# Kernel tuning notes

Measured on AMD Instinct MI355X. Metric: run time of the kernel, lower is better.

The kernel has to match this reference:

```python
import jax, jax.numpy as jnp
import numpy as np

D, E, K, H = 512, 8, 2, 128   # input_dim, num_experts, top-k, expert hidden (Expert default)
CAPF = 1.25                    # capacity_factor
N = 32768                      # tokens


def setup_inputs() -> dict:
    key = jax.random.key(0)
    ks = jax.random.split(key, 6)
    s = 0.02
    return {
        "x":  jax.random.normal(ks[0], (N, D), jnp.float32),
        "Wr": jax.random.normal(ks[1], (D, E), jnp.float32) * s,   # router linear weight
        "br": jnp.zeros((E,), jnp.float32),
        "W1": jax.random.normal(ks[2], (E, D, H), jnp.float32) * s,  # expert first linear (stacked)
        "b1": jnp.zeros((E, H), jnp.float32),
        "W2": jax.random.normal(ks[3], (E, H, D), jnp.float32) * s,  # expert second linear (stacked)
        "b2": jnp.zeros((E, D), jnp.float32),
    }


def reference(x, Wr, br, W1, b1, W2, b2):
    n = x.shape[0]
    # ---- router (eval mode: no noise, temperature=1) ----
    logits = x @ Wr + br                                   # [N, E]
    topk_vals, topk_idx = jax.lax.top_k(logits, K)         # [N, K]
    gates_k = jax.nn.softmax(topk_vals, axis=-1)
    rows = jnp.arange(n)[:, None]
    sparse_gates = jnp.zeros_like(logits).at[rows, topk_idx].set(gates_k)  # [N, E]
    confidence = topk_vals.max(axis=-1).mean()
    # ---- capacity-limited dispatch (keep first `cap` routed tokens per expert) ----
    cap = int(CAPF * (n / E))
    mask = sparse_gates > 0                                # [N, E] routed mask
    pos = jnp.cumsum(mask, axis=0) - 1                     # rank of token within expert queue
    keep = mask & (pos < cap)                              # [N, E]
    load = keep.sum(axis=0).astype(x.dtype)                # [E]
    # ---- per-expert 2-layer FFN over all tokens, combined with keep mask ----
    # (original adds expert output un-weighted by gates to kept token positions)
    h = jax.nn.relu(jnp.einsum('nd,edh->enh', x, W1) + b1[:, None, :])   # [E, N, H]
    y = jnp.einsum('enh,ehd->end', h, W2) + b2[:, None, :]               # [E, N, D]
    out = jnp.einsum('ne,end->nd', keep.astype(x.dtype), y)             # [N, D]
    # ---- load-balance stats ----
    load_dist = load / (load.sum() + 1e-8)
    load_loss = (load_dist * jnp.log(load_dist + 1e-8)).sum()
    return out, load_loss, load_dist, confidence
```

## Files before the change

### kernel.cpp

```cpp
#include <hip/hip_runtime.h>

#define D 512
#define E 8
#define H 128
#define BM 64
#define HP 136
#define RT 16

typedef __attribute__((ext_vector_type(8))) short short8v;
typedef __attribute__((ext_vector_type(4))) short short4v;
typedef __attribute__((ext_vector_type(4))) float float4v;

__device__ inline short f2bf(float f) {
  union { float f; unsigned u; } v; v.f = f;
  unsigned r = v.u + 0x7fffu + ((v.u >> 16) & 1u);
  return (short)(r >> 16);
}
__device__ inline float bf2f(short s) {
  union { unsigned u; float f; } v;
  v.u = ((unsigned)(unsigned short)s) << 16;
  return v.f;
}
__device__ inline void gload_lds4(const void* g, void* l) {
  __builtin_amdgcn_global_load_lds(
      (const __attribute__((address_space(1))) unsigned int*)g,
      (__attribute__((address_space(3))) unsigned int*)l, 4, 0, 0);
}

__global__ void k_swizzle(const float* __restrict__ W1, const float* __restrict__ W2,
                          short* __restrict__ W1f, short* __restrict__ W2f) {
  const int e = blockIdx.y;
  const int lane = threadIdx.x & 63;
  const int wv = threadIdx.x >> 6;
  const int r = lane & 15, g = lane >> 4;
  const int which = blockIdx.x >> 4;
  const int fbase = ((blockIdx.x & 15) * 4 + wv) * 2;
  if (which == 0) {
#pragma unroll
    for (int f = fbase; f < fbase + 2; ++f) {
      int ks = f >> 3, t = f & 7;
      const float* src = W1 + ((size_t)e * D + ks * 32 + g * 8) * H + t * 16 + r;
      short8v o;
#pragma unroll
      for (int j = 0; j < 8; ++j) o[j] = f2bf(src[(size_t)j * H]);
      *(short8v*)(W1f + (((size_t)e * 128 + f) * 64 + lane) * 8) = o;
    }
  } else {
#pragma unroll
    for (int f = fbase; f < fbase + 2; ++f) {
      int t = f >> 2, ks = f & 3;
      const float* src = W2 + ((size_t)e * H + ks * 32 + g * 8) * D + t * 16 + r;
      short8v o;
#pragma unroll
      for (int j = 0; j < 8; ++j) o[j] = f2bf(src[(size_t)j * D]);
      *(short8v*)(W2f + (((size_t)e * 128 + f) * 64 + lane) * 8) = o;
    }
  }
}

__global__ void k_router(const float* __restrict__ x, const float* __restrict__ Wr,
                         const float* __restrict__ br, int* __restrict__ tokE,
                         float* __restrict__ confPart, short* __restrict__ xb) {
  const int lane = threadIdx.x & 63;
  const int wave = threadIdx.x >> 6;
  const int tbase = (blockIdx.x * 4 + wave) * RT;

  float wr[8][8];
  const float4* wrp = reinterpret_cast<const float4*>(Wr) + lane * 16;
#pragma unroll
  for (int j = 0; j < 8; ++j) {
    float4 a = wrp[j * 2 + 0];
    float4 b = wrp[j * 2 + 1];
    wr[j][0] = a.x; wr[j][1] = a.y; wr[j][2] = a.z; wr[j][3] = a.w;
    wr[j][4] = b.x; wr[j][5] = b.y; wr[j][6] = b.z; wr[j][7] = b.w;
  }

  const int myE = ((lane & 1) << 2) | (lane & 2) | ((lane >> 2) & 1);
  const float brv = br[myE];

  float conf = 0.f;

#pragma unroll 2
  for (int tt = 0; tt < RT; ++tt) {
    const int token = tbase + tt;
    const float4* xp = reinterpret_cast<const float4*>(x + (size_t)token * D + lane * 8);
    float4 x0 = xp[0], x1 = xp[1];
    float xv[8] = {x0.x, x0.y, x0.z, x0.w, x1.x, x1.y, x1.z, x1.w};

    if (xb) {
      short8v p;
#pragma unroll
      for (int j = 0; j < 8; ++j) p[j] = f2bf(xv[j]);
      *(short8v*)(xb + (size_t)token * D + lane * 8) = p;
    }

    float v[8] = {0, 0, 0, 0, 0, 0, 0, 0};
#pragma unroll
    for (int j = 0; j < 8; ++j)
#pragma unroll
      for (int e = 0; e < E; ++e)
        v[e] += xv[j] * wr[j][e];

#pragma unroll
    for (int i = 0; i < 4; ++i) {
      float a = v[i] + __shfl_xor(v[i], 1, 64);
      float b = v[i + 4] + __shfl_xor(v[i + 4], 1, 64);
      v[i] = (lane & 1) ? b : a;
    }
#pragma unroll
    for (int i = 0; i < 2; ++i) {
      float a = v[i] + __shfl_xor(v[i], 2, 64);
      float b = v[i + 2] + __shfl_xor(v[i + 2], 2, 64);
      v[i] = (lane & 2) ? b : a;
    }
    {
      float a = v[0] + __shfl_xor(v[0], 4, 64);
      float b = v[1] + __shfl_xor(v[1], 4, 64);
      v[0] = (lane & 4) ? b : a;
    }
    v[0] += __shfl_xor(v[0], 8, 64);
    v[0] += __shfl_xor(v[0], 16, 64);
    v[0] += __shfl_xor(v[0], 32, 64);

    const float logit = v[0] + brv;

    float m1 = logit; int i1 = myE;
#pragma unroll
    for (int m = 1; m <= 4; m <<= 1) {
      float om = __shfl_xor(m1, m, 64);
      int oi = __shfl_xor(i1, m, 64);
      bool take = (om > m1) || (om == m1 && oi < i1);
      m1 = take ? om : m1;
      i1 = take ? oi : i1;
    }
    float s1 = (myE == i1) ? -1e30f : logit; int j1 = myE;
#pragma unroll
    for (int m = 1; m <= 4; m <<= 1) {
      float om = __shfl_xor(s1, m, 64);
      int oi = __shfl_xor(j1, m, 64);
      bool take = (om > s1) || (om == s1 && oi < j1);
      s1 = take ? om : s1;
      j1 = take ? oi : j1;
    }

    if (lane == 0) {
      tokE[token * 2 + 0] = i1;
      tokE[token * 2 + 1] = j1;
    }
    conf += m1;
  }

  __shared__ float cf[4];
  if (lane == 0) cf[wave] = conf;
  __syncthreads();
  if (threadIdx.x == 0) confPart[blockIdx.x] = cf[0] + cf[1] + cf[2] + cf[3];
}

__global__ void k_count(const int* __restrict__ tokE, int* __restrict__ chunkCnt) {
  __shared__ int c[E];
  if (threadIdx.x < E) c[threadIdx.x] = 0;
  __syncthreads();
  int token = blockIdx.x * 256 + threadIdx.x;
  atomicAdd(&c[tokE[token * 2 + 0]], 1);
  atomicAdd(&c[tokE[token * 2 + 1]], 1);
  __syncthreads();
  if (threadIdx.x < E) chunkCnt[blockIdx.x * E + threadIdx.x] = c[threadIdx.x];
}

__global__ void k_scan(const int* __restrict__ chunkCnt, const float* __restrict__ confPart,
                       int* __restrict__ chunkOff, int* __restrict__ kept,
                       float* __restrict__ outTail, int nConf, int cap, int nTok) {
  const int lane = threadIdx.x & 63;
  const int e = threadIdx.x >> 6;
  __shared__ int keptS[E];

  int v0 = chunkCnt[lane * E + e];
  int v1 = chunkCnt[(64 + lane) * E + e];
  int s0 = v0, s1 = v1;
#pragma unroll
  for (int off = 1; off < 64; off <<= 1) {
    int t0 = __shfl_up(s0, off, 64);
    int t1 = __shfl_up(s1, off, 64);
    if (lane >= off) { s0 += t0; s1 += t1; }
  }
  int tot0 = __shfl(s0, 63, 64);
  int total = tot0 + __shfl(s1, 63, 64);
  chunkOff[lane * E + e] = s0 - v0;
  chunkOff[(64 + lane) * E + e] = tot0 + s1 - v1;
  if (lane == 0) {
    int k = min(total, cap);
    kept[e] = k;
    keptS[e] = k;
  }

  __shared__ float s[512];
  float a = 0.f;
  for (int i = threadIdx.x; i < nConf; i += 512) a += confPart[i];
  s[threadIdx.x] = a;
  __syncthreads();
  for (int st = 256; st > 0; st >>= 1) {
    if (threadIdx.x < st) s[threadIdx.x] += s[threadIdx.x + st];
    __syncthreads();
  }
  if (threadIdx.x == 0) {
    float tot = 0.f, ld[E];
    for (int i = 0; i < E; ++i) { ld[i] = (float)keptS[i]; tot += ld[i]; }
    float denom = tot + 1e-8f;
    float loss = 0.f;
    for (int i = 0; i < E; ++i) {
      float dist = ld[i] / denom;
      loss += dist * logf(dist + 1e-8f);
      outTail[1 + i] = dist;
    }
    outTail[0] = loss;
    outTail[1 + E] = s[0] / (float)nTok;
  }
}

__global__ void k_dispatch(const int* __restrict__ tokE, const int* __restrict__ chunkOff,
                           int* __restrict__ expList, int2* __restrict__ tokSlot, int cap) {
  const int lane = threadIdx.x & 63;
  const int wave = threadIdx.x >> 6;
  const int token = blockIdx.x * 256 + threadIdx.x;
  const int e0 = tokE[token * 2 + 0];
  const int e1 = tokE[token * 2 + 1];
  __shared__ int wcnt[4][E];
  unsigned long long lt = (lane == 63) ? 0x7fffffffffffffffull : ((1ull << lane) - 1ull);
  int r0 = 0, r1 = 0;
#pragma unroll
  for (int e = 0; e < E; ++e) {
    unsigned long long b0 = __ballot(e0 == e);
    unsigned long long b1 = __ballot(e1 == e);
    unsigned long long m = b0 | b1;
    if (e0 == e) r0 = __popcll(m & lt);
    if (e1 == e) r1 = __popcll(m & lt);
    if (lane == 0) wcnt[wave][e] = __popcll(m);
  }
  __syncthreads();
  int base0 = chunkOff[blockIdx.x * E + e0];
  int base1 = chunkOff[blockIdx.x * E + e1];
  for (int w = 0; w < wave; ++w) {
    base0 += wcnt[w][e0];
    base1 += wcnt[w][e1];
  }
  int g0 = base0 + r0;
  int g1 = base1 + r1;
  if (g0 < cap) expList[e0 * cap + g0] = token;
  if (g1 < cap) expList[e1 * cap + g1] = token;
  tokSlot[token] = make_int2(g0 < cap ? e0 * cap + g0 : -1,
                             g1 < cap ? e1 * cap + g1 : -1);
}

template <bool USE_XB>
__global__ __launch_bounds__(256) void k_expert_mfma(
    const short* __restrict__ xb, const float* __restrict__ x,
    const short* __restrict__ W1f, const float* __restrict__ b1,
    const short* __restrict__ W2f, const float* __restrict__ b2,
    const int* __restrict__ expList, const int* __restrict__ kept,
    short* __restrict__ yscr, int cap) {
  const int e = blockIdx.y;
  const int cnt = kept[e];
  const int t0 = blockIdx.x * BM;
  if (t0 >= cnt) return;
  const int lane = threadIdx.x & 63;
  const int wave = threadIdx.x >> 6;
  const int rb = wave * 16;
  const int n15 = lane & 15;
  const int grp = lane >> 4;
  const int kg = grp * 8;

  __shared__ int toks[BM];
  __shared__ short sbuf[2 * BM * HP];

  if (threadIdx.x < BM) {
    int idx = min(t0 + (int)threadIdx.x, cnt - 1);
    toks[threadIdx.x] = expList[e * cap + idx];
  }
  __syncthreads();

  const short* w1 = W1f + (size_t)e * (128 * 512);
  const short* w2 = W2f + (size_t)e * (128 * 512);

  float4v acc[8];
#pragma unroll
  for (int t = 0; t < 8; ++t) acc[t] = (float4v){0.f, 0.f, 0.f, 0.f};

  if (USE_XB) {
    auto stageX = [&](int p) {
#pragma unroll
      for (int j = 0; j < 16; ++j) {
        int ti = wave * 16 + j;
        const short* src = xb + (size_t)toks[ti] * D + p * 128 + lane * 2;
        short* dst = &sbuf[(p & 1) * (BM * HP) + ti * HP];
        gload_lds4(src, dst);
      }
    };
    stageX(0);
    __syncthreads();
#pragma unroll
    for (int p = 0; p < 4; ++p) {
      if (p < 3) stageX(p + 1);
#pragma unroll
      for (int ksl = 0; ksl < 4; ++ksl) {
        const int ks = p * 4 + ksl;
        short8v xf = *(const short8v*)&sbuf[(p & 1) * (BM * HP) +
                                            (rb + n15) * HP + ksl * 32 + kg];
        short8v wf[8];
#pragma unroll
        for (int t = 0; t < 8; ++t)
          wf[t] = *(const short8v*)(w1 + (size_t)(ks * 8 + t) * 512 + lane * 8);
#pragma unroll
        for (int t = 0; t < 8; ++t)
          acc[t] = __builtin_amdgcn_mfma_f32_16x16x32_bf16(wf[t], xf, acc[t], 0, 0, 0);
      }
      __syncthreads();
    }
  } else {
    const float* xrowF = x + (size_t)toks[rb + n15] * D + kg;
    short8v xf[16];
#pragma unroll
    for (int ks = 0; ks < 16; ++ks) {
      float4 a = *(const float4*)(xrowF + ks * 32);
      float4 b = *(const float4*)(xrowF + ks * 32 + 4);
      short8v f;
      f[0] = f2bf(a.x); f[1] = f2bf(a.y); f[2] = f2bf(a.z); f[3] = f2bf(a.w);
      f[4] = f2bf(b.x); f[5] = f2bf(b.y); f[6] = f2bf(b.z); f[7] = f2bf(b.w);
      xf[ks] = f;
    }
#pragma unroll
    for (int ks = 0; ks < 16; ++ks) {
      short8v wf[8];
#pragma unroll
      for (int t = 0; t < 8; ++t)
        wf[t] = *(const short8v*)(w1 + (size_t)(ks * 8 + t) * 512 + lane * 8);
#pragma unroll
      for (int t = 0; t < 8; ++t)
        acc[t] = __builtin_amdgcn_mfma_f32_16x16x32_bf16(wf[t], xf[ks], acc[t], 0, 0, 0);
    }
    __syncthreads();
  }

  short* hrow = &sbuf[(rb + n15) * HP];
#pragma unroll
  for (int t = 0; t < 8; ++t) {
    float4 bb = *(const float4*)(b1 + e * H + t * 16 + grp * 4);
    short4v p;
    p[0] = f2bf(fmaxf(acc[t][0] + bb.x, 0.f));
    p[1] = f2bf(fmaxf(acc[t][1] + bb.y, 0.f));
    p[2] = f2bf(fmaxf(acc[t][2] + bb.z, 0.f));
    p[3] = f2bf(fmaxf(acc[t][3] + bb.w, 0.f));
    *(short4v*)(hrow + t * 16 + grp * 4) = p;
  }
  __syncthreads();

  short8v a4[4];
#pragma unroll
  for (int ks = 0; ks < 4; ++ks)
    a4[ks] = *(const short8v*)(&sbuf[(rb + n15) * HP + ks * 32 + kg]);

  short* yrow = yscr + ((size_t)(e * cap + t0 + rb + n15)) * D;
#pragma unroll 4
  for (int t = 0; t < 32; ++t) {
    short8v wf[4];
#pragma unroll
    for (int ks = 0; ks < 4; ++ks)
      wf[ks] = *(const short8v*)(w2 + (size_t)(t * 4 + ks) * 512 + lane * 8);
    float4v y = (float4v){0.f, 0.f, 0.f, 0.f};
#pragma unroll
    for (int ks = 0; ks < 4; ++ks)
      y = __builtin_amdgcn_mfma_f32_16x16x32_bf16(wf[ks], a4[ks], y, 0, 0, 0);
    float4 bb = *(const float4*)(b2 + e * D + t * 16 + grp * 4);
    short4v p;
    p[0] = f2bf(y[0] + bb.x);
    p[1] = f2bf(y[1] + bb.y);
    p[2] = f2bf(y[2] + bb.z);
    p[3] = f2bf(y[3] + bb.w);
    *(short4v*)(yrow + t * 16 + grp * 4) = p;
  }
}

__global__ void k_combine(const short* __restrict__ yscr, const int2* __restrict__ tokSlot,
                          float* __restrict__ out) {
  const int idx = blockIdx.x * 256 + threadIdx.x;
  const int token = idx >> 7;
  const int c4 = idx & 127;
  int2 sl = tokSlot[token];
  float4 r = make_float4(0.f, 0.f, 0.f, 0.f);
  if (sl.x >= 0) {
    short4v y = *(const short4v*)(yscr + (size_t)sl.x * D + c4 * 4);
    r.x += bf2f(y[0]); r.y += bf2f(y[1]); r.z += bf2f(y[2]); r.w += bf2f(y[3]);
  }
  if (sl.y >= 0) {
    short4v y = *(const short4v*)(yscr + (size_t)sl.y * D + c4 * 4);
    r.x += bf2f(y[0]); r.y += bf2f(y[1]); r.z += bf2f(y[2]); r.w += bf2f(y[3]);
  }
  reinterpret_cast<float4*>(out)[idx] = r;
}

extern "C" void kernel_launch(void* const* d_in, const int* in_sizes, int n_in,
                              void* d_out, int out_size, void* d_ws, size_t ws_size,
                              hipStream_t stream) {
  const float* x  = (const float*)d_in[0];
  const float* Wr = (const float*)d_in[1];
  const float* br = (const float*)d_in[2];
  const float* W1 = (const float*)d_in[3];
  const float* b1 = (const float*)d_in[4];
  const float* W2 = (const float*)d_in[5];
  const float* b2 = (const float*)d_in[6];
  float* out = (float*)d_out;

  const int N = in_sizes[0] / D;
  const int cap = (int)(1.25f * (float)(N / E));
  const int chunks = N / 256;
  const int rblocks = N / (4 * RT);

  int* tokE = (int*)d_ws;
  float* confPart = (float*)(tokE + (size_t)N * 2);
  int* chunkCnt = (int*)(confPart + rblocks);
  int* chunkOff = chunkCnt + chunks * E;
  int* kept = chunkOff + chunks * E;
  int2* tokSlot = (int2*)(kept + E);
  int* expList = (int*)(tokSlot + N);
  short* W1f = (short*)(expList + (size_t)E * cap);
  short* W2f = W1f + (size_t)E * H * D;
  short* yscr = W2f + (size_t)E * H * D;
  short* xb = yscr + (size_t)E * cap * D;

  const size_t needed = (size_t)((char*)(xb + (size_t)N * D) - (char*)d_ws);
  const bool useXB = ws_size >= needed;

  k_swizzle<<<dim3(32, E), 256, 0, stream>>>(W1, W2, W1f, W2f);

  k_router<<<rblocks, 256, 0, stream>>>(x, Wr, br, tokE, confPart,
                                        useXB ? xb : nullptr);
  k_count<<<chunks, 256, 0, stream>>>(tokE, chunkCnt);
  k_scan<<<1, 512, 0, stream>>>(chunkCnt, confPart, chunkOff, kept,
                                out + (size_t)N * D, rblocks, cap, N);
  k_dispatch<<<chunks, 256, 0, stream>>>(tokE, chunkOff, expList, tokSlot, cap);

  const int tiles = (cap + BM - 1) / BM;
  dim3 g5(tiles, E);
  if (useXB)
    k_expert_mfma<true><<<g5, 256, 0, stream>>>(xb, x, W1f, b1, W2f, b2,
                                                expList, kept, yscr, cap);
  else
    k_expert_mfma<false><<<g5, 256, 0, stream>>>(nullptr, x, W1f, b1, W2f, b2,
                                                 expList, kept, yscr, cap);

  k_combine<<<(N * D / 4) / 256, 256, 0, stream>>>(yscr, tokSlot, out);
}
```

Before: 113.3 us.

## Enlarge expert tile to 128 tokens with a 2x4 wave grid for weight reuse

The expert FFN kernel now processes 128 tokens per block with 512 threads. The 8 waves form a 2x4 grid: each wave covers 64 rows and a quarter of the hidden/output columns. Each W1/W2 fragment loaded from global is therefore reused across several 16-row tiles, cutting weight traffic per token. The trade-off is half as many blocks (fewer than two per CU), a larger LDS footprint and one-block-per-CU launch bounds, so occupancy and latency hiding may suffer. RT is also changed for the router stage.

```diff
diff --git a/kernel.cpp b/kernel.cpp
--- a/kernel.cpp
+++ b/kernel.cpp
@@ -3,9 +3,9 @@
 #define D 512
 #define E 8
 #define H 128
-#define BM 64
+#define BM 128
 #define HP 136
-#define RT 16
+#define RT 8
 
 typedef __attribute__((ext_vector_type(8))) short short8v;
 typedef __attribute__((ext_vector_type(4))) short short4v;
@@ -252,7 +252,7 @@
 }
 
 template <bool USE_XB>
-__global__ __launch_bounds__(256) void k_expert_mfma(
+__global__ __launch_bounds__(512, 1) void k_expert_mfma(
     const short* __restrict__ xb, const float* __restrict__ x,
     const short* __restrict__ W1f, const float* __restrict__ b1,
     const short* __restrict__ W2f, const float* __restrict__ b2,
@@ -264,7 +264,8 @@
   if (t0 >= cnt) return;
   const int lane = threadIdx.x & 63;
   const int wave = threadIdx.x >> 6;
-  const int rb = wave * 16;
+  const int rowg = wave >> 2;
+  const int ng = wave & 3;
   const int n15 = lane & 15;
   const int grp = lane >> 4;
   const int kg = grp * 8;
@@ -281,9 +282,12 @@
   const short* w1 = W1f + (size_t)e * (128 * 512);
   const short* w2 = W2f + (size_t)e * (128 * 512);
 
-  float4v acc[8];
-#pragma unroll
-  for (int t = 0; t < 8; ++t) acc[t] = (float4v){0.f, 0.f, 0.f, 0.f};
+  float4v acc[4][2];
+#pragma unroll
+  for (int r = 0; r < 4; ++r)
+#pragma unroll
+    for (int t = 0; t < 2; ++t)
+      acc[r][t] = (float4v){0.f, 0.f, 0.f, 0.f};
 
   if (USE_XB) {
     auto stageX = [&](int p) {
@@ -303,79 +307,105 @@
 #pragma unroll
       for (int ksl = 0; ksl < 4; ++ksl) {
         const int ks = p * 4 + ksl;
-        short8v xf = *(const short8v*)&sbuf[(p & 1) * (BM * HP) +
-                                            (rb + n15) * HP + ksl * 32 + kg];
-        short8v wf[8];
-#pragma unroll
-        for (int t = 0; t < 8; ++t)
-          wf[t] = *(const short8v*)(w1 + (size_t)(ks * 8 + t) * 512 + lane * 8);
-#pragma unroll
-        for (int t = 0; t < 8; ++t)
-          acc[t] = __builtin_amdgcn_mfma_f32_16x16x32_bf16(wf[t], xf, acc[t], 0, 0, 0);
+        const short* sb = &sbuf[(p & 1) * (BM * HP)];
+        short8v xf[4];
+#pragma unroll
+        for (int r = 0; r < 4; ++r)
+          xf[r] = *(const short8v*)&sb[(rowg * 64 + r * 16 + n15) * HP + ksl * 32 + kg];
+        short8v wf[2];
+#pragma unroll
+        for (int t = 0; t < 2; ++t)
+          wf[t] = *(const short8v*)(w1 + (size_t)(ks * 8 + ng * 2 + t) * 512 + lane * 8);
+#pragma unroll
+        for (int t = 0; t < 2; ++t)
+#pragma unroll
+          for (int r = 0; r < 4; ++r)
+            acc[r][t] = __builtin_amdgcn_mfma_f32_16x16x32_bf16(wf[t], xf[r], acc[r][t], 0, 0, 0);
       }
       __syncthreads();
     }
   } else {
-    const float* xrowF = x + (size_t)toks[rb + n15] * D + kg;
-    short8v xf[16];
-#pragma unroll
+#pragma unroll 1
     for (int ks = 0; ks < 16; ++ks) {
-      float4 a = *(const float4*)(xrowF + ks * 32);
-      float4 b = *(const float4*)(xrowF + ks * 32 + 4);
-      short8v f;
-      f[0] = f2bf(a.x); f[1] = f2bf(a.y); f[2] = f2bf(a.z); f[3] = f2bf(a.w);
-      f[4] = f2bf(b.x); f[5] = f2bf(b.y); f[6] = f2bf(b.z); f[7] = f2bf(b.w);
-      xf[ks] = f;
-    }
-#pragma unroll
-    for (int ks = 0; ks < 16; ++ks) {
-      short8v wf[8];
-#pragma unroll
-      for (int t = 0; t < 8; ++t)
-        wf[t] = *(const short8v*)(w1 + (size_t)(ks * 8 + t) * 512 + lane * 8);
-#pragma unroll
-      for (int t = 0; t < 8; ++t)
-        acc[t] = __builtin_amdgcn_mfma_f32_16x16x32_bf16(wf[t], xf[ks], acc[t], 0, 0, 0);
+      short8v xf[4];
+#pragma unroll
+      for (int r = 0; r < 4; ++r) {
+        const float* xr = x + (size_t)toks[rowg * 64 + r * 16 + n15] * D + kg + ks * 32;
+        float4 a0 = *(const float4*)(xr);
+        float4 a1 = *(const float4*)(xr + 4);
+        short8v f;
+        f[0] = f2bf(a0.x); f[1] = f2bf(a0.y); f[2] = f2bf(a0.z); f[3] = f2bf(a0.w);
+        f[4] = f2bf(a1.x); f[5] = f2bf(a1.y); f[6] = f2bf(a1.z); f[7] = f2bf(a1.w);
+        xf[r] = f;
+      }
+      short8v wf[2];
+#pragma unroll
+      for (int t = 0; t < 2; ++t)
+        wf[t] = *(const short8v*)(w1 + (size_t)(ks * 8 + ng * 2 + t) * 512 + lane * 8);
+#pragma unroll
+      for (int t = 0; t < 2; ++t)
+#pragma unroll
+        for (int r = 0; r < 4; ++r)
+          acc[r][t] = __builtin_amdgcn_mfma_f32_16x16x32_bf16(wf[t], xf[r], acc[r][t], 0, 0, 0);
     }
     __syncthreads();
   }
 
-  short* hrow = &sbuf[(rb + n15) * HP];
-#pragma unroll
-  for (int t = 0; t < 8; ++t) {
-    float4 bb = *(const float4*)(b1 + e * H + t * 16 + grp * 4);
-    short4v p;
-    p[0] = f2bf(fmaxf(acc[t][0] + bb.x, 0.f));
-    p[1] = f2bf(fmaxf(acc[t][1] + bb.y, 0.f));
-    p[2] = f2bf(fmaxf(acc[t][2] + bb.z, 0.f));
-    p[3] = f2bf(fmaxf(acc[t][3] + bb.w, 0.f));
-    *(short4v*)(hrow + t * 16 + grp * 4) = p;
-  }
-  __syncthreads();
-
-  short8v a4[4];
-#pragma unroll
-  for (int ks = 0; ks < 4; ++ks)
-    a4[ks] = *(const short8v*)(&sbuf[(rb + n15) * HP + ks * 32 + kg]);
-
-  short* yrow = yscr + ((size_t)(e * cap + t0 + rb + n15)) * D;
+#pragma unroll
+  for (int t = 0; t < 2; ++t) {
+    int tg = ng * 2 + t;
+    float4 bb = *(const float4*)(b1 + e * H + tg * 16 + grp * 4);
+#pragma unroll
+    for (int r = 0; r < 4; ++r) {
+      short4v p;
+      p[0] = f2bf(fmaxf(acc[r][t][0] + bb.x, 0.f));
+      p[1] = f2bf(fmaxf(acc[r][t][1] + bb.y, 0.f));
+      p[2] = f2bf(fmaxf(acc[r][t][2] + bb.z, 0.f));
+      p[3] = f2bf(fmaxf(acc[r][t][3] + bb.w, 0.f));
+      *(short4v*)(&sbuf[(rowg * 64 + r * 16 + n15) * HP + tg * 16 + grp * 4]) = p;
+    }
+  }
+  __syncthreads();
+
+#pragma unroll
+  for (int rp = 0; rp < 2; ++rp) {
+    const int rbase = rowg * 64 + rp * 32;
+    short8v a4[2][4];
+#pragma unroll
+    for (int ri = 0; ri < 2; ++ri)
+#pragma unroll
+      for (int ks = 0; ks < 4; ++ks)
+        a4[ri][ks] = *(const short8v*)(&sbuf[(rbase + ri * 16 + n15) * HP + ks * 32 + kg]);
+
+    short* yrow0 = yscr + ((size_t)(e * cap + t0 + rbase + n15)) * D;
+    short* yrow1 = yrow0 + (size_t)16 * D;
 #pragma unroll 4
-  for (int t = 0; t < 32; ++t) {
-    short8v wf[4];
-#pragma unroll
-    for (int ks = 0; ks < 4; ++ks)
-      wf[ks] = *(const short8v*)(w2 + (size_t)(t * 4 + ks) * 512 + lane * 8);
-    float4v y = (float4v){0.f, 0.f, 0.f, 0.f};
-#pragma unroll
-    for (int ks = 0; ks < 4; ++ks)
-      y = __builtin_amdgcn_mfma_f32_16x16x32_bf16(wf[ks], a4[ks], y, 0, 0, 0);
-    float4 bb = *(const float4*)(b2 + e * D + t * 16 + grp * 4);
-    short4v p;
-    p[0] = f2bf(y[0] + bb.x);
-    p[1] = f2bf(y[1] + bb.y);
-    p[2] = f2bf(y[2] + bb.z);
-    p[3] = f2bf(y[3] + bb.w);
-    *(short4v*)(yrow + t * 16 + grp * 4) = p;
+    for (int tt = 0; tt < 8; ++tt) {
+      const int t = ng * 8 + tt;
+      short8v wf[4];
+#pragma unroll
+      for (int ks = 0; ks < 4; ++ks)
+        wf[ks] = *(const short8v*)(w2 + (size_t)(t * 4 + ks) * 512 + lane * 8);
+      float4v y0 = (float4v){0.f, 0.f, 0.f, 0.f};
+      float4v y1 = (float4v){0.f, 0.f, 0.f, 0.f};
+#pragma unroll
+      for (int ks = 0; ks < 4; ++ks) {
+        y0 = __builtin_amdgcn_mfma_f32_16x16x32_bf16(wf[ks], a4[0][ks], y0, 0, 0, 0);
+        y1 = __builtin_amdgcn_mfma_f32_16x16x32_bf16(wf[ks], a4[1][ks], y1, 0, 0, 0);
+      }
+      float4 bb = *(const float4*)(b2 + e * D + t * 16 + grp * 4);
+      short4v p0, p1;
+      p0[0] = f2bf(y0[0] + bb.x);
+      p0[1] = f2bf(y0[1] + bb.y);
+      p0[2] = f2bf(y0[2] + bb.z);
+      p0[3] = f2bf(y0[3] + bb.w);
+      p1[0] = f2bf(y1[0] + bb.x);
+      p1[1] = f2bf(y1[1] + bb.y);
+      p1[2] = f2bf(y1[2] + bb.z);
+      p1[3] = f2bf(y1[3] + bb.w);
+      *(short4v*)(yrow0 + t * 16 + grp * 4) = p0;
+      *(short4v*)(yrow1 + t * 16 + grp * 4) = p1;
+    }
   }
 }
 
@@ -441,10 +471,10 @@
   const int tiles = (cap + BM - 1) / BM;
   dim3 g5(tiles, E);
   if (useXB)
-    k_expert_mfma<true><<<g5, 256, 0, stream>>>(xb, x, W1f, b1, W2f, b2,
+    k_expert_mfma<true><<<g5, 512, 0, stream>>>(xb, x, W1f, b1, W2f, b2,
                                                 expList, kept, yscr, cap);
   else
-    k_expert_mfma<false><<<g5, 256, 0, stream>>>(nullptr, x, W1f, b1, W2f, b2,
+    k_expert_mfma<false><<<g5, 512, 0, stream>>>(nullptr, x, W1f, b1, W2f, b2,
                                                  expList, kept, yscr, cap);
 
   k_combine<<<(N * D / 4) / 256, 256, 0, stream>>>(yscr, tokSlot, out);
```

New measurement: 105.5 us. -6.8%, faster.
